# Optimization experiments

Hardware: AMD Instinct MI355X
Metric: run time of the kernel (lower is better)

## Reference

```python
import jax, jax.numpy as jnp
import numpy as np

B, N, K, NUM_CLASSES = 8, 4096, 20, 40


def _knn_idx(x, k):
    # x: [B, N, D] -> indices of k nearest neighbors (self excluded), [B, N, k]
    sq = jnp.sum(x * x, axis=-1)  # [B, N]
    dist = sq[:, :, None] + sq[:, None, :] - 2.0 * jnp.einsum('bnd,bmd->bnm', x, x)
    dist = jnp.where(jnp.eye(x.shape[1], dtype=bool)[None], jnp.inf, dist)
    return jax.lax.top_k(-dist, k)[1]


def _edge_conv(x, idx, params):
    # PyG EdgeConv with max aggregation: max_j MLP([x_i, x_j - x_i])
    x_j = jax.vmap(lambda xb, ib: xb[ib])(x, idx)              # [B, N, K, D]
    x_i = jnp.broadcast_to(x[:, :, None, :], x_j.shape)        # [B, N, K, D]
    h = jnp.concatenate([x_i, x_j - x_i], axis=-1)             # [B, N, K, 2D]
    for w, b in params:
        h = jax.nn.relu(h @ w + b)
    return jnp.max(h, axis=2)                                  # [B, N, out]


def setup_inputs() -> dict:
    key = jax.random.key(0)
    ks = jax.random.split(key, 12)

    def lin(k, i, o):  # torch Linear default init
        k1, k2 = jax.random.split(k)
        s = 1.0 / np.sqrt(i)
        return (jax.random.uniform(k1, (i, o), jnp.float32, -s, s),
                jax.random.uniform(k2, (o,), jnp.float32, -s, s))

    inp = {
        'pos': jax.random.normal(ks[0], (B * N, 3), jnp.float32),
        'batch': jnp.repeat(jnp.arange(B, dtype=jnp.int32), N),
    }
    names = [('m1w1', 'm1b1', 6, 64), ('m1w2', 'm1b2', 64, 64), ('m1w3', 'm1b3', 64, 64),
             ('m2w1', 'm2b1', 128, 128), ('m2w2', 'm2b2', 128, 128), ('m2w3', 'm2b3', 128, 256),
             ('lin0_w', 'lin0_b', 256, 512), ('lin1_w', 'lin1_b', 512, 256),
             ('lin2_w', 'lin2_b', 256, 256), ('lin3_w', 'lin3_b', 256, NUM_CLASSES)]
    for t, (wn, bn, i, o) in enumerate(names):
        w, b = lin(ks[t + 1], i, o)
        inp[wn] = w
        inp[bn] = b
    return inp


def reference(pos, batch, m1w1, m1b1, m1w2, m1b2, m1w3, m1b3,
              m2w1, m2b1, m2w2, m2b2, m2w3, m2b3,
              lin0_w, lin0_b, lin1_w, lin1_b, lin2_w, lin2_b, lin3_w, lin3_b):
    x = pos.reshape(B, N, 3)
    x = _edge_conv(x, _knn_idx(x, K), [(m1w1, m1b1), (m1w2, m1b2), (m1w3, m1b3)])   # [B,N,64]
    x = _edge_conv(x, _knn_idx(x, K), [(m2w1, m2b1), (m2w2, m2b2), (m2w3, m2b3)])   # [B,N,256]
    x = jax.nn.relu(x @ lin0_w + lin0_b)                                            # [B,N,512]
    x = jax.ops.segment_max(x.reshape(B * N, -1), batch, num_segments=B)            # [B,512]
    x = jax.nn.relu(x @ lin1_w + lin1_b)
    x = jax.nn.relu(x @ lin2_w + lin2_b)   # dropout is identity in eval mode
    x = x @ lin3_w + lin3_b
    return jax.nn.log_softmax(x, axis=-1)
```

## Files before the change

### kernel.cpp

```cpp
#include <hip/hip_runtime.h>

#define DEVI static __device__ __forceinline__

typedef __attribute__((ext_vector_type(4))) float f32x4;
typedef __attribute__((ext_vector_type(8))) short short8;
typedef __attribute__((ext_vector_type(4))) short short4v;
typedef __attribute__((ext_vector_type(8))) __bf16 bf16x8;

#define N_    4096
#define KNN_  20
#define NPTS  32768

DEVI unsigned short f2bf(float f){
  unsigned u = __float_as_uint(f);
  u += 0x7FFFu + ((u >> 16) & 1u);
  return (unsigned short)(u >> 16);
}
DEVI float bf2f(unsigned short s){ return __uint_as_float(((unsigned)s) << 16); }
DEVI float bf2fs(short s){ return __uint_as_float(((unsigned)(unsigned short)s) << 16); }
DEVI unsigned umin32(unsigned a, unsigned b){ return a < b ? a : b; }
DEVI unsigned umax32(unsigned a, unsigned b){ return a > b ? a : b; }

DEVI f32x4 mfma16(short8 a, short8 b, f32x4 c){
  return __builtin_amdgcn_mfma_f32_16x16x32_bf16(
      __builtin_bit_cast(bf16x8, a), __builtin_bit_cast(bf16x8, b), c, 0, 0, 0);
}

DEVI short8 lds_frag(const unsigned short* buf, int row, int k0, int strideS, int swzMask){
  return *(const short8*)(buf + row*strideS + (k0 ^ ((row & swzMask) << 3)));
}
DEVI void lds_put8(unsigned short* buf, int row, int k0, int strideS, int swzMask, short8 v){
  *(short8*)(buf + row*strideS + (k0 ^ ((row & swzMask) << 3))) = v;
}

DEVI void ins32(unsigned K, unsigned (&a)[20]){
#pragma unroll
  for (int t = 19; t >= 1; --t) a[t] = umin32(a[t], umax32(a[t-1], K));
  a[0] = umin32(a[0], K);
}
DEVI void ins64(double K, double (&a)[20]){
#pragma unroll
  for (int t = 19; t >= 1; --t) a[t] = fmin(a[t], fmax(a[t-1], K));
  a[0] = fmin(a[0], K);
}

DEVI void stage_body(const float* __restrict__ src, unsigned short* __restrict__ dh,
                     unsigned short* __restrict__ dl, int K, int Nw, int KT, int lblk){
  int tid = lblk*256 + (int)threadIdx.x;
  int l = tid & 63;
  int kk = (tid >> 6) % KT;
  int nt = tid / (64*KT);
  int n = nt*16 + (l & 15);
  int kb = kk*32 + ((l >> 4) << 3);
#pragma unroll
  for (int e=0;e<8;++e){
    int k = kb + e;
    float w = (k < K) ? src[(size_t)k*Nw + n] : 0.f;
    unsigned short h = f2bf(w);
    dh[(size_t)tid*8 + e] = h;
    if (dl) dl[(size_t)tid*8 + e] = f2bf(w - bf2f(h));
  }
}

__global__ __launch_bounds__(256) void stage_all_k(const float* __restrict__ pos,
    unsigned short* __restrict__ p3h, unsigned short* __restrict__ p3l, float* __restrict__ nrm3,
    const float* __restrict__ m1w1, const float* __restrict__ m1w2, const float* __restrict__ m1w3,
    const float* __restrict__ m2w1, const float* __restrict__ m2w2, const float* __restrict__ m2w3,
    const float* __restrict__ l0w,
    unsigned short* __restrict__ W1h, unsigned short* __restrict__ W1l,
    unsigned short* __restrict__ W2h, unsigned short* __restrict__ W2l,
    unsigned short* __restrict__ W3h, unsigned short* __restrict__ W3l,
    unsigned short* __restrict__ V1, unsigned short* __restrict__ V2, unsigned short* __restrict__ V3,
    unsigned short* __restrict__ W0){
  const int blk = blockIdx.x;
  if (blk < 128){
    int p = blk*256 + (int)threadIdx.x;
    float x = pos[(size_t)p*3], y = pos[(size_t)p*3+1], z = pos[(size_t)p*3+2];
    float v[8] = {x, y, z, 0.f, 0.f, 0.f, 0.f, 0.f};
#pragma unroll
    for (int c = 0; c < 8; ++c){
      unsigned short h = f2bf(v[c]);
      p3h[(size_t)p*8 + c] = h;
      p3l[(size_t)p*8 + c] = f2bf(v[c] - bf2f(h));
    }
    nrm3[p] = fmaf(x, x, fmaf(y, y, z*z));
    return;
  }
  int b = blk - 128;
  if      (b < 1)  stage_body(m1w1, W1h, W1l, 6,   64,  1, b);
  else if (b < 3)  stage_body(m1w2, W2h, W2l, 64,  64,  2, b-1);
  else if (b < 5)  stage_body(m1w3, W3h, W3l, 64,  64,  2, b-3);
  else if (b < 13) stage_body(m2w1, V1, nullptr, 128, 128, 4, b-5);
  else if (b < 21) stage_body(m2w2, V2, nullptr, 128, 128, 4, b-13);
  else if (b < 37) stage_body(m2w3, V3, nullptr, 128, 256, 4, b-21);
  else             stage_body(l0w,  W0, nullptr, 256, 512, 8, b-37);
}

template<int MODE>
__global__ __launch_bounds__(256) void knn_k(const unsigned short* __restrict__ Xh,
                                             const unsigned short* __restrict__ Xl,
                                             const float* __restrict__ nrm,
                                             unsigned* __restrict__ pk){
  __shared__ __align__(16) char smem[15616];
  unsigned* buf    = (unsigned*)(smem);
  unsigned* rowThr = (unsigned*)(smem + 6144);
  unsigned* mD     = (unsigned*)(smem);

  const int blk = blockIdx.x;
  const int rt = blk & 63, ch = (blk >> 6) & 1, bb = blk >> 7;
  const int rowbase = rt * 64, cbase = ch * 2048;
  const size_t gb = (size_t)bb * N_;
  const int tid = threadIdx.x, lane = tid & 63, wid = tid >> 6;
  const int l15 = lane & 15, g = lane >> 4, kL = g << 3, r0 = g << 2;
  const int qidx = wid*16 + l15;

  if (tid < 64) rowThr[tid] = 0xFFFFFFFFu;

  short8 qh0 = {0,0,0,0,0,0,0,0}, qh1 = {0,0,0,0,0,0,0,0};
  short8 ql0 = {0,0,0,0,0,0,0,0}, ql1 = {0,0,0,0,0,0,0,0};
  if (MODE == 1){
    const size_t ab = (gb + rowbase + qidx) * 64;
    qh0 = *(const short8*)(Xh + ab + kL);
    qh1 = *(const short8*)(Xh + ab + 32 + kL);
    ql0 = *(const short8*)(Xl + ab + kL);
    ql1 = *(const short8*)(Xl + ab + 32 + kL);
  } else {
    if (g == 0){
      const size_t ab = (gb + rowbase + qidx) * 8;
      qh0 = *(const short8*)(Xh + ab);
      ql0 = *(const short8*)(Xl + ab);
    }
  }
  const float si = nrm[gb + rowbase + qidx];

  unsigned arr[20];
#pragma unroll
  for (int t = 0; t < 20; ++t) arr[t] = 0xFFFFFFFFu;
  int cnt = 0;
  bool selfR[4];
#pragma unroll
  for (int r = 0; r < 4; ++r) selfR[r] = (l15 == r0 + r);

  __syncthreads();

  for (int c = 0; c < 32; ++c){
    const bool selfTile = (cbase + c*64 == rowbase);
    unsigned kb16[16];
#pragma unroll
    for (int ct = 0; ct < 4; ++ct){
      f32x4 acc = {0.f,0.f,0.f,0.f};
      if (MODE == 1){
        const size_t cb64 = (gb + cbase + c*64 + ct*16 + l15) * 64;
        short8 ch0 = *(const short8*)(Xh + cb64 + kL);
        short8 ch1 = *(const short8*)(Xh + cb64 + 32 + kL);
        short8 cl0 = *(const short8*)(Xl + cb64 + kL);
        short8 cl1 = *(const short8*)(Xl + cb64 + 32 + kL);
        acc = mfma16(ch0, qh0, acc); acc = mfma16(ch1, qh1, acc);
        acc = mfma16(cl0, qh0, acc); acc = mfma16(cl1, qh1, acc);
        acc = mfma16(ch0, ql0, acc); acc = mfma16(ch1, ql1, acc);
      } else {
        short8 cb = {0,0,0,0,0,0,0,0}, cl_ = {0,0,0,0,0,0,0,0};
        if (g == 0){
          const size_t cb8 = (size_t)(gb + cbase + c*64 + ct*16 + l15) * 8;
          cb  = *(const short8*)(Xh + cb8);
          cl_ = *(const short8*)(Xl + cb8);
        }
        acc = mfma16(cb,  qh0, acc);
        acc = mfma16(cl_, qh0, acc);
        acc = mfma16(cb,  ql0, acc);
      }
      f32x4 sj4 = *(const f32x4*)(nrm + gb + cbase + c*64 + ct*16 + r0);
#pragma unroll
      for (int r = 0; r < 4; ++r){
        unsigned cid = (unsigned)(c*64 + ct*16 + r0 + r);
        float dv = fmaxf(fmaf(-2.f, acc[r], si + sj4[r]), 0.f);
        unsigned kb = (__float_as_uint(dv) & ~0x7FFu) | cid;
        if (selfTile && ct == wid && selfR[r]) kb = 0x7F800000u | cid;
        kb16[ct*4 + r] = kb;
      }
    }
    {
      unsigned thrP = rowThr[qidx];
#pragma unroll
      for (int i = 0; i < 16; ++i){
        unsigned kb = kb16[i];
        if (kb < thrP){
          if (cnt < 6){ buf[cnt*256 + tid] = kb; ++cnt; }
          else ins32(kb, arr);
        }
      }
      for (int t = 0; t < cnt; ++t) ins32(buf[t*256 + tid], arr);
      cnt = 0;
      atomicMin(&rowThr[qidx], arr[19]);
    }
  }
  __syncthreads();
  if (g > 0){
#pragma unroll
    for (int t = 0; t < 20; ++t) mD[(qidx*3 + g-1)*20 + t] = arr[t];
  }
  __syncthreads();
  if (g == 0){
    for (int gg = 0; gg < 3; ++gg)
#pragma unroll
      for (int t = 0; t < 20; ++t) ins32(mD[(qidx*3 + gg)*20 + t], arr);
    const size_t gp = gb + rowbase + qidx;
#pragma unroll
    for (int t = 0; t < 20; ++t) pk[((size_t)(ch*20 + t))*NPTS + gp] = arr[t];
  }
}

__global__ __launch_bounds__(256) void knn_merge_k(const unsigned* __restrict__ pk,
                                                   int* __restrict__ idx){
  const int p = blockIdx.x*256 + threadIdx.x;
  double arr[20];
#pragma unroll
  for (int t = 0; t < 20; ++t){
    unsigned k = pk[(size_t)t*NPTS + p];
    unsigned long long K = (((unsigned long long)(k & ~0x7FFu)) << 1) | (k & 0x7FFu);
    arr[t] = __builtin_bit_cast(double, K);
  }
#pragma unroll
  for (int t = 0; t < 20; ++t){
    unsigned k = pk[(size_t)(20 + t)*NPTS + p];
    unsigned long long K = (((unsigned long long)(k & ~0x7FFu)) << 1) | (2048u + (k & 0x7FFu));
    ins64(__builtin_bit_cast(double, K), arr);
  }
  int* o = idx + (size_t)p*KNN_;
#pragma unroll
  for (int t = 0; t < 20; ++t)
    o[t] = (int)(__builtin_bit_cast(unsigned long long, arr[t]) & 0xFFFu);
}

__global__ __launch_bounds__(256) void ec1_k(const float* __restrict__ pos, const int* __restrict__ idx1,
    const unsigned short* __restrict__ W1h, const unsigned short* __restrict__ W1l,
    const unsigned short* __restrict__ W2h, const unsigned short* __restrict__ W2l,
    const unsigned short* __restrict__ W3h, const unsigned short* __restrict__ W3l,
    const float* __restrict__ b1, const float* __restrict__ b2, const float* __restrict__ b3,
    unsigned short* __restrict__ x1h, unsigned short* __restrict__ x1l, float* __restrict__ nrm1){
  __shared__ __align__(16) char smem[51200];
  unsigned short* Ah  = (unsigned short*)(smem);
  unsigned short* Al  = (unsigned short*)(smem + 5120);
  unsigned short* H1h = (unsigned short*)(smem + 10240);
  unsigned short* H1l = (unsigned short*)(smem + 20480);
  unsigned short* H2h = (unsigned short*)(smem + 30720);
  unsigned short* H2l = (unsigned short*)(smem + 40960);
  float* dump = (float*)(smem);
  const int p0 = blockIdx.x * 4;
  const int bb = p0 >> 12;
  const int tid = threadIdx.x, lane = tid & 63, wid = tid >> 6;
  const int l15 = lane & 15, g = lane >> 4, r0 = g << 2;

  if (tid < 80){
    int p = p0 + tid/20, slot = tid%20;
    int j = idx1[(size_t)p*KNN_ + slot];
    int gj = (bb << 12) + j;
    float a6[6];
    a6[0] = pos[(size_t)p*3]; a6[1] = pos[(size_t)p*3+1]; a6[2] = pos[(size_t)p*3+2];
    a6[3] = pos[(size_t)gj*3]   - a6[0];
    a6[4] = pos[(size_t)gj*3+1] - a6[1];
    a6[5] = pos[(size_t)gj*3+2] - a6[2];
    int mt = tid >> 4, lrow = tid & 15;
    short8 vh, vl, zz = {0,0,0,0,0,0,0,0};
#pragma unroll
    for (int c=0;c<8;++c){
      float v = (c < 6) ? a6[c] : 0.f;
      unsigned short h = f2bf(v);
      vh[c] = (short)h;
      vl[c] = (short)f2bf(v - bf2f(h));
    }
    *(short8*)(Ah + (mt*64 + lrow)*8) = vh;
    *(short8*)(Al + (mt*64 + lrow)*8) = vl;
#pragma unroll
    for (int gg=1;gg<4;++gg){
      *(short8*)(Ah + (mt*64 + gg*16 + lrow)*8) = zz;
      *(short8*)(Al + (mt*64 + gg*16 + lrow)*8) = zz;
    }
  }
  __syncthreads();
  const int nt = wid;
  const int kk2 = nt >> 1, sub2 = (nt & 1)*2 + (g >> 1), e0 = (g & 1)*4;
  {
    short8 wh = *(const short8*)(W1h + ((size_t)nt*64 + lane)*8);
    short8 wl = *(const short8*)(W1l + ((size_t)nt*64 + lane)*8);
    f32x4 b4 = *(const f32x4*)(b1 + nt*16 + r0);
    for (int mt=0; mt<5; ++mt){
      short8 ah = *(const short8*)(Ah + (mt*64 + lane)*8);
      short8 al = *(const short8*)(Al + (mt*64 + lane)*8);
      f32x4 acc = {0.f,0.f,0.f,0.f};
      acc = mfma16(wh, ah, acc);
      acc = mfma16(wl, ah, acc);
      acc = mfma16(wh, al, acc);
      short4v vh4, vl4;
#pragma unroll
      for (int r=0;r<4;++r){
        float v = fmaxf(acc[r] + b4[r], 0.f);
        unsigned short h = f2bf(v);
        vh4[r] = (short)h;
        vl4[r] = (short)f2bf(v - bf2f(h));
      }
      *(short4v*)(H1h + ((mt*2 + kk2)*64 + sub2*16 + l15)*8 + e0) = vh4;
      *(short4v*)(H1l + ((mt*2 + kk2)*64 + sub2*16 + l15)*8 + e0) = vl4;
    }
  }
  __syncthreads();
  {
    short8 wh0 = *(const short8*)(W2h + ((size_t)(nt*2+0)*64 + lane)*8);
    short8 wh1 = *(const short8*)(W2h + ((size_t)(nt*2+1)*64 + lane)*8);
    short8 wl0 = *(const short8*)(W2l + ((size_t)(nt*2+0)*64 + lane)*8);
    short8 wl1 = *(const short8*)(W2l + ((size_t)(nt*2+1)*64 + lane)*8);
    f32x4 b4 = *(const f32x4*)(b2 + nt*16 + r0);
    for (int mt=0; mt<5; ++mt){
      short8 ah0 = *(const short8*)(H1h + ((mt*2+0)*64 + lane)*8);
      short8 ah1 = *(const short8*)(H1h + ((mt*2+1)*64 + lane)*8);
      short8 al0 = *(const short8*)(H1l + ((mt*2+0)*64 + lane)*8);
      short8 al1 = *(const short8*)(H1l + ((mt*2+1)*64 + lane)*8);
      f32x4 acc = {0.f,0.f,0.f,0.f};
      acc = mfma16(wh0, ah0, acc); acc = mfma16(wh1, ah1, acc);
      acc = mfma16(wl0, ah0, acc); acc = mfma16(wl1, ah1, acc);
      acc = mfma16(wh0, al0, acc); acc = mfma16(wh1, al1, acc);
      short4v vh4, vl4;
#pragma unroll
      for (int r=0;r<4;++r){
        float v = fmaxf(acc[r] + b4[r], 0.f);
        unsigned short h = f2bf(v);
        vh4[r] = (short)h;
        vl4[r] = (short)f2bf(v - bf2f(h));
      }
      *(short4v*)(H2h + ((mt*2 + kk2)*64 + sub2*16 + l15)*8 + e0) = vh4;
      *(short4v*)(H2l + ((mt*2 + kk2)*64 + sub2*16 + l15)*8 + e0) = vl4;
    }
  }
  __syncthreads();
  {
    short8 wh0 = *(const short8*)(W3h + ((size_t)(nt*2+0)*64 + lane)*8);
    short8 wh1 = *(const short8*)(W3h + ((size_t)(nt*2+1)*64 + lane)*8);
    short8 wl0 = *(const short8*)(W3l + ((size_t)(nt*2+0)*64 + lane)*8);
    short8 wl1 = *(const short8*)(W3l + ((size_t)(nt*2+1)*64 + lane)*8);
    f32x4 b4 = *(const f32x4*)(b3 + nt*16 + r0);
    for (int mt=0; mt<5; ++mt){
      short8 ah0 = *(const short8*)(H2h + ((mt*2+0)*64 + lane)*8);
      short8 ah1 = *(const short8*)(H2h + ((mt*2+1)*64 + lane)*8);
      short8 al0 = *(const short8*)(H2l + ((mt*2+0)*64 + lane)*8);
      short8 al1 = *(const short8*)(H2l + ((mt*2+1)*64 + lane)*8);
      f32x4 acc = {0.f,0.f,0.f,0.f};
      acc = mfma16(wh0, ah0, acc); acc = mfma16(wh1, ah1, acc);
      acc = mfma16(wl0, ah0, acc); acc = mfma16(wl1, ah1, acc);
      acc = mfma16(wh0, al0, acc); acc = mfma16(wh1, al1, acc);
      f32x4 o;
#pragma unroll
      for (int r=0;r<4;++r) o[r] = fmaxf(acc[r] + b4[r], 0.f);
      int edge = mt*16 + l15;
      *(f32x4*)(dump + edge*68 + nt*16 + r0) = o;
    }
  }
  __syncthreads();
  if (tid < 64){
    int p = tid >> 4, c4 = tid & 15;
    int st = tid % 20;
    float mx[4] = {0.f,0.f,0.f,0.f};
    for (int e=0;e<20;++e){
      int ee = st + e; if (ee >= 20) ee -= 20;
      f32x4 v = *(const f32x4*)(dump + (p*20 + ee)*68 + c4*4);
#pragma unroll
      for (int r=0;r<4;++r) mx[r] = fmaxf(mx[r], v[r]);
    }
    int gp = p0 + p;
    short4v h4, l4;
    float s = 0.f;
#pragma unroll
    for (int r=0;r<4;++r){
      float m = mx[r];
      unsigned short h = f2bf(m);
      h4[r] = (short)h;
      l4[r] = (short)f2bf(m - bf2f(h));
      s = fmaf(m, m, s);
    }
    *(short4v*)(x1h + (size_t)gp*64 + c4*4) = h4;
    *(short4v*)(x1l + (size_t)gp*64 + c4*4) = l4;
    s += __shfl_xor(s, 1); s += __shfl_xor(s, 2); s += __shfl_xor(s, 4); s += __shfl_xor(s, 8);
    if (c4 == 0) nrm1[gp] = s;
  }
}

__global__ __launch_bounds__(256) void ec2_k(const unsigned short* __restrict__ x1h, const int* __restrict__ idx2,
    const unsigned short* __restrict__ V1, const unsigned short* __restrict__ V2, const unsigned short* __restrict__ V3,
    const float* __restrict__ b1, const float* __restrict__ b2, const float* __restrict__ b3,
    unsigned short* __restrict__ x2b){
  __shared__ __align__(16) char smem[81920];
  unsigned short* A  = (unsigned short*)(smem);
  unsigned short* H1 = (unsigned short*)(smem + 40960);
  const int p0 = blockIdx.x * 8, bb = p0 >> 12;
  const int tid = threadIdx.x, lane = tid & 63, wid = tid >> 6;
  const int l15 = lane & 15, r0 = (lane >> 4) << 2;

  if (tid < 160){
    int p = p0 + tid/20, slot = tid%20;
    int j = idx2[(size_t)p*KNN_ + slot];
    int gj = (bb << 12) + j;
    const unsigned short* xi = x1h + (size_t)p*64;
    const unsigned short* xj = x1h + (size_t)gj*64;
    int mt = tid >> 4, lrow = tid & 15;
#pragma unroll
    for (int q=0;q<8;++q){
      short8 vi = *(const short8*)(xi + q*8);
      short8 vj = *(const short8*)(xj + q*8);
      short8 vd;
#pragma unroll
      for (int c=0;c<8;++c) vd[c] = (short)f2bf(bf2fs(vj[c]) - bf2fs(vi[c]));
      *(short8*)(A + (((mt*4 + (q>>2))*64) + (q&3)*16 + lrow)*8) = vi;
      *(short8*)(A + (((mt*4 + 2 + (q>>2))*64) + (q&3)*16 + lrow)*8) = vd;
    }
  }
  __syncthreads();

  {
    short8 w[2][4];
#pragma unroll
    for (int ni=0;ni<2;++ni)
#pragma unroll
      for (int kk=0;kk<4;++kk)
        w[ni][kk] = *(const short8*)(V1 + ((size_t)((wid*2+ni)*4+kk)*64 + lane)*8);
    f32x4 b4[2];
    b4[0] = *(const f32x4*)(b1 + (wid*2+0)*16 + r0);
    b4[1] = *(const f32x4*)(b1 + (wid*2+1)*16 + r0);
    for (int mt=0; mt<10; ++mt){
      short8 bfr[4];
#pragma unroll
      for (int kk=0;kk<4;++kk) bfr[kk] = *(const short8*)(A + ((mt*4+kk)*64 + lane)*8);
#pragma unroll
      for (int ni=0;ni<2;++ni){
        int nt = wid*2 + ni;
        f32x4 acc = {0.f,0.f,0.f,0.f};
#pragma unroll
        for (int kk=0;kk<4;++kk) acc = mfma16(w[ni][kk], bfr[kk], acc);
        short4v v4;
#pragma unroll
        for (int r=0;r<4;++r) v4[r] = (short)f2bf(fmaxf(acc[r] + b4[ni][r], 0.f));
        int kk2 = nt >> 1, sub2 = (nt & 1)*2 + (r0 >> 3);
        *(short4v*)(H1 + ((mt*4+kk2)*64 + sub2*16 + l15)*8 + (r0 & 4)) = v4;
      }
    }
  }
  __syncthreads();
  {
    short8 w[2][4];
#pragma unroll
    for (int ni=0;ni<2;++ni)
#pragma unroll
      for (int kk=0;kk<4;++kk)
        w[ni][kk] = *(const short8*)(V2 + ((size_t)((wid*2+ni)*4+kk)*64 + lane)*8);
    f32x4 b4[2];
    b4[0] = *(const f32x4*)(b2 + (wid*2+0)*16 + r0);
    b4[1] = *(const f32x4*)(b2 + (wid*2+1)*16 + r0);
    for (int mt=0; mt<10; ++mt){
      short8 bfr[4];
#pragma unroll
      for (int kk=0;kk<4;++kk) bfr[kk] = *(const short8*)(H1 + ((mt*4+kk)*64 + lane)*8);
#pragma unroll
      for (int ni=0;ni<2;++ni){
        int nt = wid*2 + ni;
        f32x4 acc = {0.f,0.f,0.f,0.f};
#pragma unroll
        for (int kk=0;kk<4;++kk) acc = mfma16(w[ni][kk], bfr[kk], acc);
        short4v v4;
#pragma unroll
        for (int r=0;r<4;++r) v4[r] = (short)f2bf(fmaxf(acc[r] + b4[ni][r], 0.f));
        int kk2 = nt >> 1, sub2 = (nt & 1)*2 + (r0 >> 3);
        *(short4v*)(A + ((mt*4+kk2)*64 + sub2*16 + l15)*8 + (r0 & 4)) = v4;
      }
    }
  }
  __syncthreads();
  for (int g2=0; g2<2; ++g2){
    {
      short8 w[2][4];
#pragma unroll
      for (int ni=0;ni<2;++ni)
#pragma unroll
        for (int kk=0;kk<4;++kk)
          w[ni][kk] = *(const short8*)(V3 + ((size_t)((g2*8 + wid*2+ni)*4+kk)*64 + lane)*8);
      f32x4 b4[2];
      b4[0] = *(const f32x4*)(b3 + (g2*8 + wid*2+0)*16 + r0);
      b4[1] = *(const f32x4*)(b3 + (g2*8 + wid*2+1)*16 + r0);
      for (int mt=0; mt<10; ++mt){
        short8 bfr[4];
#pragma unroll
        for (int kk=0;kk<4;++kk) bfr[kk] = *(const short8*)(A + ((mt*4+kk)*64 + lane)*8);
#pragma unroll
        for (int ni=0;ni<2;++ni){
          int ntl = wid*2 + ni;
          f32x4 acc = {0.f,0.f,0.f,0.f};
#pragma unroll
          for (int kk=0;kk<4;++kk) acc = mfma16(w[ni][kk], bfr[kk], acc);
          short4v v4;
#pragma unroll
          for (int r=0;r<4;++r) v4[r] = (short)f2bf(fmaxf(acc[r] + b4[ni][r], 0.f));
          int kk2 = ntl >> 1, sub2 = (ntl & 1)*2 + (r0 >> 3);
          *(short4v*)(H1 + ((mt*4+kk2)*64 + sub2*16 + l15)*8 + (r0 & 4)) = v4;
        }
      }
    }
    __syncthreads();
    if (tid < 128){
      int p = tid >> 4, c8 = tid & 15;
      int kk = c8 >> 2, sub = c8 & 3;
      unsigned short mx[8];
#pragma unroll
      for (int e=0;e<8;++e) mx[e] = 0;
      for (int e=0;e<20;++e){
        int ee = e + p + c8; ee -= (ee >= 20) ? 20 : 0; ee -= (ee >= 20) ? 20 : 0;
        int row = p*20 + ee;
        short8 v = *(const short8*)(H1 + (((row>>4)*4 + kk)*64 + sub*16 + (row & 15))*8);
#pragma unroll
        for (int k2=0;k2<8;++k2){
          unsigned short u = (unsigned short)v[k2];
          mx[k2] = u > mx[k2] ? u : mx[k2];
        }
      }
      short8 o;
#pragma unroll
      for (int k2=0;k2<8;++k2) o[k2] = (short)mx[k2];
      *(short8*)(x2b + (size_t)(p0 + p)*256 + g2*128 + c8*8) = o;
    }
    __syncthreads();
  }
}

__global__ __launch_bounds__(256) void lin0_k(const unsigned short* __restrict__ x2b, const unsigned short* __restrict__ W0s,
                                              const float* __restrict__ b0, unsigned* __restrict__ pool){
  __shared__ __align__(16) char smem[67584];
  unsigned short* A = (unsigned short*)(smem);
  unsigned* ploc = (unsigned*)(smem + 65536);
  const int blk = blockIdx.x; const size_t row0 = (size_t)blk * 128; const int bb = blk >> 5;
  const int tid = threadIdx.x, lane = tid & 63, wid = tid >> 6;
  for (int it = tid; it < 4096; it += 256){
    int row = it >> 5, q = (it & 31) << 3;
    lds_put8(A, row, q, 256, 7, *(const short8*)(x2b + (row0 + row)*256 + q));
  }
  ploc[tid] = 0u; ploc[tid+256] = 0u;
  __syncthreads();
  const int l15 = lane & 15, kL = (lane >> 4) << 3;
  short8 af[2][8];
#pragma unroll
  for (int m=0;m<2;++m)
#pragma unroll
    for (int kk=0;kk<8;++kk)
      af[m][kk] = lds_frag(A, (wid*2+m)*16 + l15, kk*32 + kL, 256, 7);
  for (int nt=0; nt<32; ++nt){
    f32x4 a0 = {0.f,0.f,0.f,0.f}, a1 = {0.f,0.f,0.f,0.f};
#pragma unroll
    for (int kk=0;kk<8;++kk){
      short8 w = *(const short8*)(W0s + ((size_t)(nt*8+kk)*64 + lane)*8);
      a0 = mfma16(af[0][kk], w, a0);
      a1 = mfma16(af[1][kk], w, a1);
    }
    int col = nt*16 + l15;
    float m = fmaxf(fmaxf(fmaxf(a0[0],a0[1]),fmaxf(a0[2],a0[3])),
                    fmaxf(fmaxf(a1[0],a1[1]),fmaxf(a1[2],a1[3])));
    m = fmaxf(m + b0[col], 0.f);
    atomicMax(&ploc[col], __float_as_uint(m));
  }
  __syncthreads();
  atomicMax(&pool[(size_t)bb*512 + tid], ploc[tid]);
  atomicMax(&pool[(size_t)bb*512 + tid + 256], ploc[tid+256]);
}

__global__ __launch_bounds__(256) void head8_k(const unsigned* __restrict__ pool,
    const float* __restrict__ w1, const float* __restrict__ bb1,
    const float* __restrict__ w2, const float* __restrict__ bb2,
    const float* __restrict__ w3, const float* __restrict__ bb3,
    float* __restrict__ out){
  __shared__ float pl[512];
  __shared__ float y1[256];
  __shared__ float y2[256];
  __shared__ float lg[40];
  const int row = blockIdx.x;
  const int tid = threadIdx.x;
  for (int it = tid; it < 512; it += 256) pl[it] = __uint_as_float(pool[row*512 + it]);
  __syncthreads();
  {
    float acc = bb1[tid];
    for (int k=0;k<512;++k) acc = fmaf(pl[k], w1[(size_t)k*256 + tid], acc);
    y1[tid] = fmaxf(acc, 0.f);
  }
  __syncthreads();
  {
    float acc = bb2[tid];
    for (int k=0;k<256;++k) acc = fmaf(y1[k], w2[(size_t)k*256 + tid], acc);
    y2[tid] = fmaxf(acc, 0.f);
  }
  __syncthreads();
  if (tid < 40){
    float acc = bb3[tid];
    for (int k=0;k<256;++k) acc = fmaf(y2[k], w3[(size_t)k*40 + tid], acc);
    lg[tid] = acc;
  }
  __syncthreads();
  if (tid < 40){
    float m = -__builtin_inff();
    for (int c2=0;c2<40;++c2) m = fmaxf(m, lg[c2]);
    float s = 0.f;
    for (int c2=0;c2<40;++c2) s += expf(lg[c2] - m);
    out[row*40 + tid] = lg[tid] - m - logf(s);
  }
}

extern "C" void kernel_launch(void* const* d_in, const int* in_sizes, int n_in,
                              void* d_out, int out_size, void* d_ws, size_t ws_size,
                              hipStream_t stream){
  (void)in_sizes; (void)n_in; (void)out_size; (void)ws_size;
  const float* pos  = (const float*)d_in[0];
  const float* m1w1 = (const float*)d_in[2];  const float* m1b1 = (const float*)d_in[3];
  const float* m1w2 = (const float*)d_in[4];  const float* m1b2 = (const float*)d_in[5];
  const float* m1w3 = (const float*)d_in[6];  const float* m1b3 = (const float*)d_in[7];
  const float* m2w1 = (const float*)d_in[8];  const float* m2b1 = (const float*)d_in[9];
  const float* m2w2 = (const float*)d_in[10]; const float* m2b2 = (const float*)d_in[11];
  const float* m2w3 = (const float*)d_in[12]; const float* m2b3 = (const float*)d_in[13];
  const float* l0w  = (const float*)d_in[14]; const float* l0b  = (const float*)d_in[15];
  const float* l1w  = (const float*)d_in[16]; const float* l1b  = (const float*)d_in[17];
  const float* l2w  = (const float*)d_in[18]; const float* l2b  = (const float*)d_in[19];
  const float* l3w  = (const float*)d_in[20]; const float* l3b  = (const float*)d_in[21];

  char* ws = (char*)d_ws;
  size_t o = 0;
  auto alloc = [&](size_t bytes){ size_t r = o; o += (bytes + 255) & ~(size_t)255; return r; };
  size_t o_idx1 = alloc((size_t)NPTS*20*4);
  size_t o_idx2 = alloc((size_t)NPTS*20*4);
  size_t o_x1h  = alloc((size_t)NPTS*64*2);
  size_t o_x1l  = alloc((size_t)NPTS*64*2);
  size_t o_nrm  = alloc((size_t)NPTS*4);
  size_t o_x2b  = alloc((size_t)NPTS*256*2);
  size_t o_pool = alloc(8*512*4);
  size_t o_p3h  = alloc((size_t)NPTS*8*2);
  size_t o_p3l  = alloc((size_t)NPTS*8*2);
  size_t o_nrm3 = alloc((size_t)NPTS*4);
  size_t o_pk   = alloc((size_t)2*20*NPTS*4);
  size_t o_W1h = alloc(4*1*64*8*2),  o_W1l = alloc(4*1*64*8*2);
  size_t o_W2h = alloc(4*2*64*8*2),  o_W2l = alloc(4*2*64*8*2);
  size_t o_W3h = alloc(4*2*64*8*2),  o_W3l = alloc(4*2*64*8*2);
  size_t o_V1  = alloc(8*4*64*8*2);
  size_t o_V2  = alloc(8*4*64*8*2);
  size_t o_V3  = alloc(16*4*64*8*2);
  size_t o_W0  = alloc(32*8*64*8*2);

  hipMemsetAsync(ws + o_pool, 0, 8*512*4, stream);

  stage_all_k<<<229,256,0,stream>>>(pos,
      (unsigned short*)(ws+o_p3h), (unsigned short*)(ws+o_p3l), (float*)(ws+o_nrm3),
      m1w1, m1w2, m1w3, m2w1, m2w2, m2w3, l0w,
      (unsigned short*)(ws+o_W1h), (unsigned short*)(ws+o_W1l),
      (unsigned short*)(ws+o_W2h), (unsigned short*)(ws+o_W2l),
      (unsigned short*)(ws+o_W3h), (unsigned short*)(ws+o_W3l),
      (unsigned short*)(ws+o_V1), (unsigned short*)(ws+o_V2), (unsigned short*)(ws+o_V3),
      (unsigned short*)(ws+o_W0));

  knn_k<0><<<1024,256,0,stream>>>((const unsigned short*)(ws+o_p3h), (const unsigned short*)(ws+o_p3l),
                                  (const float*)(ws+o_nrm3), (unsigned*)(ws+o_pk));
  knn_merge_k<<<128,256,0,stream>>>((const unsigned*)(ws+o_pk), (int*)(ws+o_idx1));

  ec1_k<<<8192,256,0,stream>>>(pos, (const int*)(ws+o_idx1),
      (const unsigned short*)(ws+o_W1h), (const unsigned short*)(ws+o_W1l),
      (const unsigned short*)(ws+o_W2h), (const unsigned short*)(ws+o_W2l),
      (const unsigned short*)(ws+o_W3h), (const unsigned short*)(ws+o_W3l),
      m1b1, m1b2, m1b3,
      (unsigned short*)(ws+o_x1h), (unsigned short*)(ws+o_x1l), (float*)(ws+o_nrm));

  knn_k<1><<<1024,256,0,stream>>>((const unsigned short*)(ws+o_x1h), (const unsigned short*)(ws+o_x1l),
                                  (const float*)(ws+o_nrm), (unsigned*)(ws+o_pk));
  knn_merge_k<<<128,256,0,stream>>>((const unsigned*)(ws+o_pk), (int*)(ws+o_idx2));

  ec2_k<<<4096,256,0,stream>>>((const unsigned short*)(ws+o_x1h), (const int*)(ws+o_idx2),
      (const unsigned short*)(ws+o_V1), (const unsigned short*)(ws+o_V2), (const unsigned short*)(ws+o_V3),
      m2b1, m2b2, m2b3, (unsigned short*)(ws+o_x2b));

  lin0_k<<<256,256,0,stream>>>((const unsigned short*)(ws+o_x2b), (const unsigned short*)(ws+o_W0),
                               l0b, (unsigned*)(ws+o_pool));

  head8_k<<<8,256,0,stream>>>((const unsigned*)(ws+o_pool), l1w, l1b, l2w, l2b, l3w, l3b, (float*)d_out);
}
```

Before: 691.5 us.

## Stage kNN candidate tiles in double-buffered LDS with register prefetch

The kNN kernel now copies each 64-point candidate tile (high/low bf16 features and norms) into shared memory once per block, double-buffered. The next tile is prefetched into registers while the current one is processed, and a barrier follows each tile. Before, every wave loaded the same candidate data from global memory. The key construction is also reordered so the threshold comparison runs on raw distance bits and the candidate id and self-exclusion are applied only to entries that pass. This adds LDS pressure (about 39 KB in mode 1) and a per-iteration barrier, both of which may reduce occupancy.

```diff
diff --git a/kernel.cpp b/kernel.cpp
--- a/kernel.cpp
+++ b/kernel.cpp
@@ -101,10 +101,19 @@
                                              const unsigned short* __restrict__ Xl,
                                              const float* __restrict__ nrm,
                                              unsigned* __restrict__ pk){
-  __shared__ __align__(16) char smem[15616];
-  unsigned* buf    = (unsigned*)(smem);
-  unsigned* rowThr = (unsigned*)(smem + 6144);
-  unsigned* mD     = (unsigned*)(smem);
+  constexpr int BSTR = MODE ? 4096 : 512;
+  constexpr int OBL  = MODE ? 16384 : 2048;
+  constexpr int OBUF = MODE ? 32768 : 4096;
+  constexpr int OTHR = OBUF + 6144;
+  constexpr int OSQ  = OTHR + 256;
+  constexpr int SM   = MODE ? (OSQ + 512) : 15360;
+  __shared__ __align__(16) char smem[SM];
+  unsigned short* BhA = (unsigned short*)(smem);
+  unsigned short* BlA = (unsigned short*)(smem + OBL);
+  unsigned* buf      = (unsigned*)(smem + OBUF);
+  unsigned* rowThr   = (unsigned*)(smem + OTHR);
+  float* sqjA        = (float*)(smem + OSQ);
+  unsigned* mD       = (unsigned*)(smem);
 
   const int blk = blockIdx.x;
   const int rt = blk & 63, ch = (blk >> 6) & 1, bb = blk >> 7;
@@ -141,50 +150,91 @@
 #pragma unroll
   for (int r = 0; r < 4; ++r) selfR[r] = (l15 == r0 + r);
 
+  if (MODE == 1){
+    for (int f = tid; f < 512; f += 256){
+      int lf = f & 63, half = (f >> 6) & 1, ct = f >> 7;
+      int row = ct*16 + (lf & 15);
+      int col = half*32 + ((lf >> 4) << 3);
+      const size_t src = (gb + cbase + row) * 64 + col;
+      *(short8*)(BhA + f*8) = *(const short8*)(Xh + src);
+      *(short8*)(BlA + f*8) = *(const short8*)(Xl + src);
+    }
+  } else {
+    if (tid < 64)       *(short8*)(BhA + tid*8)      = *(const short8*)(Xh + (gb + cbase + tid)*8);
+    else if (tid < 128) *(short8*)(BlA + (tid-64)*8) = *(const short8*)(Xl + (gb + cbase + (tid-64))*8);
+  }
+  if (tid < 64) sqjA[tid] = nrm[gb + cbase + tid];
   __syncthreads();
 
   for (int c = 0; c < 32; ++c){
+    const int cur = c & 1;
+    const unsigned short* Bh = BhA + cur*BSTR;
+    const unsigned short* Bl = BlA + cur*BSTR;
+    const float* sqj = sqjA + cur*64;
     const bool selfTile = (cbase + c*64 == rowbase);
+    const bool more = (c + 1 < 32);
+
+    short8 nh0 = {0,0,0,0,0,0,0,0}, nh1 = {0,0,0,0,0,0,0,0};
+    short8 nl0 = {0,0,0,0,0,0,0,0}, nl1 = {0,0,0,0,0,0,0,0};
+    float nsq = 0.f;
+    if (more){
+      if (MODE == 1){
+#pragma unroll
+        for (int ff = 0; ff < 2; ++ff){
+          int f = tid + ff*256;
+          int lf = f & 63, half = (f >> 6) & 1, ct = f >> 7;
+          int row = ct*16 + (lf & 15);
+          int col = half*32 + ((lf >> 4) << 3);
+          const size_t src = (gb + cbase + (c+1)*64 + row) * 64 + col;
+          if (ff == 0){ nh0 = *(const short8*)(Xh + src); nl0 = *(const short8*)(Xl + src); }
+          else        { nh1 = *(const short8*)(Xh + src); nl1 = *(const short8*)(Xl + src); }
+        }
+      } else {
+        if (tid < 64)       nh0 = *(const short8*)(Xh + (gb + cbase + (c+1)*64 + tid)*8);
+        else if (tid < 128) nl0 = *(const short8*)(Xl + (gb + cbase + (c+1)*64 + (tid-64))*8);
+      }
+      if (tid < 64) nsq = nrm[gb + cbase + (c+1)*64 + tid];
+    }
+
     unsigned kb16[16];
 #pragma unroll
     for (int ct = 0; ct < 4; ++ct){
       f32x4 acc = {0.f,0.f,0.f,0.f};
       if (MODE == 1){
-        const size_t cb64 = (gb + cbase + c*64 + ct*16 + l15) * 64;
-        short8 ch0 = *(const short8*)(Xh + cb64 + kL);
-        short8 ch1 = *(const short8*)(Xh + cb64 + 32 + kL);
-        short8 cl0 = *(const short8*)(Xl + cb64 + kL);
-        short8 cl1 = *(const short8*)(Xl + cb64 + 32 + kL);
+        const int fb = lane*8;
+        short8 ch0 = *(const short8*)(Bh + (ct*2+0)*512 + fb);
+        short8 ch1 = *(const short8*)(Bh + (ct*2+1)*512 + fb);
+        short8 cl0 = *(const short8*)(Bl + (ct*2+0)*512 + fb);
+        short8 cl1 = *(const short8*)(Bl + (ct*2+1)*512 + fb);
         acc = mfma16(ch0, qh0, acc); acc = mfma16(ch1, qh1, acc);
         acc = mfma16(cl0, qh0, acc); acc = mfma16(cl1, qh1, acc);
         acc = mfma16(ch0, ql0, acc); acc = mfma16(ch1, ql1, acc);
       } else {
         short8 cb = {0,0,0,0,0,0,0,0}, cl_ = {0,0,0,0,0,0,0,0};
         if (g == 0){
-          const size_t cb8 = (size_t)(gb + cbase + c*64 + ct*16 + l15) * 8;
-          cb  = *(const short8*)(Xh + cb8);
-          cl_ = *(const short8*)(Xl + cb8);
+          cb  = *(const short8*)(Bh + (ct*16 + l15)*8);
+          cl_ = *(const short8*)(Bl + (ct*16 + l15)*8);
         }
         acc = mfma16(cb,  qh0, acc);
         acc = mfma16(cl_, qh0, acc);
         acc = mfma16(cb,  ql0, acc);
       }
-      f32x4 sj4 = *(const f32x4*)(nrm + gb + cbase + c*64 + ct*16 + r0);
+      f32x4 sj4 = *(const f32x4*)(sqj + ct*16 + r0);
 #pragma unroll
       for (int r = 0; r < 4; ++r){
-        unsigned cid = (unsigned)(c*64 + ct*16 + r0 + r);
         float dv = fmaxf(fmaf(-2.f, acc[r], si + sj4[r]), 0.f);
-        unsigned kb = (__float_as_uint(dv) & ~0x7FFu) | cid;
-        if (selfTile && ct == wid && selfR[r]) kb = 0x7F800000u | cid;
-        kb16[ct*4 + r] = kb;
-      }
-    }
+        kb16[ct*4 + r] = __float_as_uint(dv);
+      }
+    }
+
     {
-      unsigned thrP = rowThr[qidx];
+      unsigned thrUp = rowThr[qidx] | 0x7FFu;
 #pragma unroll
       for (int i = 0; i < 16; ++i){
-        unsigned kb = kb16[i];
-        if (kb < thrP){
+        unsigned b = kb16[i];
+        if (b <= thrUp){
+          if (selfTile && (i >> 2) == wid && selfR[i & 3]) continue;
+          unsigned kb = (b & ~0x7FFu) | (unsigned)(c*64 + (i >> 2)*16 + r0 + (i & 3));
           if (cnt < 6){ buf[cnt*256 + tid] = kb; ++cnt; }
           else ins32(kb, arr);
         }
@@ -193,6 +243,22 @@
       cnt = 0;
       atomicMin(&rowThr[qidx], arr[19]);
     }
+
+    if (more){
+      unsigned short* BhN = BhA + (cur^1)*BSTR;
+      unsigned short* BlN = BlA + (cur^1)*BSTR;
+      if (MODE == 1){
+        *(short8*)(BhN + tid*8)       = nh0;
+        *(short8*)(BhN + (tid+256)*8) = nh1;
+        *(short8*)(BlN + tid*8)       = nl0;
+        *(short8*)(BlN + (tid+256)*8) = nl1;
+      } else {
+        if (tid < 64)       *(short8*)(BhN + tid*8)      = nh0;
+        else if (tid < 128) *(short8*)(BlN + (tid-64)*8) = nl0;
+      }
+      if (tid < 64) sqjA[(cur^1)*64 + tid] = nsq;
+    }
+    __syncthreads();
   }
   __syncthreads();
   if (g > 0){
```

Result: faster. 575.8 us (-16.7%).
